# Performance work log

Hardware: AMD Instinct MI355X
Metric: run time of the kernel (lower is better)

The kernel has to match this reference:

```python
import jax, jax.numpy as jnp
import numpy as np

N_NODES = 50000


def setup_inputs() -> dict:
    key = jax.random.key(0)
    ks = jax.random.split(key, 6)
    d_in, d_out = 256, 256
    n_edges = 1_600_000
    x = jax.random.normal(ks[0], (N_NODES, d_in), dtype=jnp.float32)
    edge_index = jax.random.randint(ks[1], (2, n_edges), 0, N_NODES, dtype=jnp.int64)
    edge_attr = jax.random.normal(ks[2], (n_edges, 16), dtype=jnp.float32)  # unused by forward
    W1 = jax.random.normal(ks[3], (d_in, d_out), dtype=jnp.float32) * (1.0 / np.sqrt(d_in))
    b1 = jnp.zeros((d_out,), dtype=jnp.float32)
    W2 = jax.random.normal(ks[4], (d_out, d_out), dtype=jnp.float32) * (1.0 / np.sqrt(d_out))
    b2 = jnp.zeros((d_out,), dtype=jnp.float32)
    eps = jnp.zeros((1,), dtype=jnp.float32)  # train_eps=True, init 0
    return {"x": x, "edge_index": edge_index, "edge_attr": edge_attr,
            "W1": W1, "b1": b1, "W2": W2, "b2": b2, "eps": eps}


def reference(x, edge_index, edge_attr, W1, b1, W2, b2, eps):
    src, dst = edge_index[0], edge_index[1]
    # sum aggregation: agg[i] = sum_{(j->i) in E} x[j]
    agg = jax.ops.segment_sum(x[src], dst, num_segments=N_NODES)  # [N, d_in]
    h = (1.0 + eps[0]) * x + agg
    # MLP: Linear -> ReLU -> (dropout=0) -> Linear
    h = jax.nn.relu(h @ W1 + b1)
    out = h @ W2 + b2
    return out
```

## Files before the change

kernel.cpp:

```cpp
#include <hip/hip_runtime.h>
#include <stdint.h>

#define NODES 50000
#define D 256
#define MP 50048
#define NBUCK 196
#define CAP 10240
#define EPB 4096
#define HS_LD 264
#define CAST_BLOCKS 12500

typedef short bf16x8 __attribute__((ext_vector_type(8)));
typedef float f32x4 __attribute__((ext_vector_type(4)));

__device__ inline unsigned short f2b(float f) {
    unsigned int u = __float_as_uint(f);
    unsigned int r = (u + 0x7fffu + ((u >> 16) & 1u)) >> 16;
    return (unsigned short)r;
}

__device__ inline bool ei_is64(const int* ei) {
    return (ei[1] | ei[3] | ei[5] | ei[7]) == 0;
}
__device__ inline int ei_get(const int* __restrict__ ei, long long pos, bool is64) {
    return is64 ? ei[2 * pos] : ei[(int)pos];
}

__global__ __launch_bounds__(256) void prep_kernel(const float* __restrict__ x,
                                                   unsigned short* __restrict__ xb,
                                                   int* __restrict__ bcnt,
                                                   const float* __restrict__ W1,
                                                   const float* __restrict__ W2,
                                                   unsigned short* __restrict__ P1,
                                                   unsigned short* __restrict__ P2,
                                                   int* __restrict__ offs, int E) {
    int blk = blockIdx.x;
    if (blk < CAST_BLOCKS) {
        if (blk == 0 && threadIdx.x < NBUCK) bcnt[threadIdx.x] = 0;
        if (blk == 0 && threadIdx.x == 0) offs[NODES] = E;
        int t = blk * 256 + threadIdx.x;
        float4 v = ((const float4*)x)[t];
        unsigned int lo = (unsigned int)f2b(v.x) | ((unsigned int)f2b(v.y) << 16);
        unsigned int hi = (unsigned int)f2b(v.z) | ((unsigned int)f2b(v.w) << 16);
        ((uint2*)xb)[t] = make_uint2(lo, hi);
    } else {
        int t = (blk - CAST_BLOCKS) * 256 + threadIdx.x;
        const float* W = (t < 8192) ? W1 : W2;
        unsigned short* P = (t < 8192) ? P1 : P2;
        int u = t & 8191;
        int lane = u & 63, nt = (u >> 6) & 15, s = u >> 10;
        int q = lane >> 4, n = nt * 16 + (lane & 15);
        int kbase = s * 32 + q * 8;
#pragma unroll
        for (int j = 0; j < 8; j++) P[u * 8 + j] = f2b(W[(kbase + j) * D + n]);
    }
}

__global__ __launch_bounds__(256) void partA_kernel(const int* __restrict__ ei, int E,
                                                    int* __restrict__ bcnt,
                                                    unsigned int* __restrict__ ebufT) {
    __shared__ int cnt[256];
    __shared__ int gbase[256];
    __shared__ int lcur[256];
    bool is64 = ei_is64(ei);
    int tid = threadIdx.x;
    cnt[tid] = 0;
    lcur[tid] = 0;
    __syncthreads();
    long long pairBase = ((long long)blockIdx.x * EPB) >> 1;
    unsigned int w[16];
    int bk[16];
#pragma unroll
    for (int r = 0; r < 8; r++) {
        long long pp = pairBase + (long long)r * 256 + tid;
        long long e0 = pp * 2;
        int s0 = 0, s1 = 0, d0 = 0, d1 = 0;
        bool v1 = (e0 + 1 < E), v0 = (e0 < E);
        if (v1) {
            if (is64) {
                uint4 sv = *(const uint4*)(ei + 4 * pp);
                uint4 dv = *(const uint4*)(ei + (size_t)2 * E + 4 * pp);
                s0 = (int)sv.x; s1 = (int)sv.z; d0 = (int)dv.x; d1 = (int)dv.z;
            } else {
                uint2 sv = *(const uint2*)(ei + 2 * pp);
                uint2 dv = *(const uint2*)(ei + (size_t)E + 2 * pp);
                s0 = (int)sv.x; s1 = (int)sv.y; d0 = (int)dv.x; d1 = (int)dv.y;
            }
        } else if (v0) {
            s0 = ei_get(ei, e0, is64);
            d0 = ei_get(ei, (long long)E + e0, is64);
        }
        bk[2 * r] = v0 ? (d0 >> 8) : -1;
        bk[2 * r + 1] = v1 ? (d1 >> 8) : -1;
        w[2 * r] = ((unsigned int)(d0 & 255) << 16) | (unsigned int)s0;
        w[2 * r + 1] = ((unsigned int)(d1 & 255) << 16) | (unsigned int)s1;
        if (v0) atomicAdd(&cnt[bk[2 * r]], 1);
        if (v1) atomicAdd(&cnt[bk[2 * r + 1]], 1);
    }
    __syncthreads();
    if (tid < NBUCK && cnt[tid] > 0) gbase[tid] = atomicAdd(&bcnt[tid], cnt[tid]);
    __syncthreads();
#pragma unroll
    for (int r = 0; r < 16; r++) {
        if (bk[r] >= 0) {
            int p = atomicAdd(&lcur[bk[r]], 1);
            ebufT[(size_t)bk[r] * CAP + gbase[bk[r]] + p] = w[r];
        }
    }
}

__global__ __launch_bounds__(1024) void partB_kernel(const int* __restrict__ bcnt,
                                                     const unsigned int* __restrict__ ebufT,
                                                     int* __restrict__ offs,
                                                     int* __restrict__ ebuf) {
    __shared__ int sb[256];
    __shared__ int ncnt[2048];
    __shared__ int ncur[2048];
    __shared__ int nexcl[256];
    int b = blockIdx.x, tid = threadIdx.x;
    if (tid < 256) sb[tid] = (tid < NBUCK) ? bcnt[tid] : 0;
    for (int i = tid; i < 2048; i += 1024) ncnt[i] = 0;
    __syncthreads();
    for (int off = 1; off < 256; off <<= 1) {
        int xv = 0;
        if (tid < 256 && tid >= off) xv = sb[tid - off];
        __syncthreads();
        if (tid < 256) sb[tid] += xv;
        __syncthreads();
    }
    int n = bcnt[b];
    int base = sb[b] - n;
    const unsigned int* reg = ebufT + (size_t)b * CAP;
    for (int i = tid; i < n; i += 1024) {
        unsigned int w = reg[i];
        atomicAdd(&ncnt[((w >> 16) << 3) | ((w & 0xffffu) >> 13)], 1);
    }
    __syncthreads();
    if (tid < 256) {
        int s = 0;
#pragma unroll
        for (int c = 0; c < 8; c++) s += ncnt[tid * 8 + c];
        nexcl[tid] = s;
    }
    __syncthreads();
    for (int off = 1; off < 256; off <<= 1) {
        int xv = 0;
        if (tid < 256 && tid >= off) xv = nexcl[tid - off];
        __syncthreads();
        if (tid < 256) nexcl[tid] += xv;
        __syncthreads();
    }
    if (tid < 256) {
        int s = 0;
#pragma unroll
        for (int c = 0; c < 8; c++) s += ncnt[tid * 8 + c];
        int excl = nexcl[tid] - s;
        int node = b * 256 + tid;
        if (node < NODES) offs[node] = base + excl;
        int run = excl;
#pragma unroll
        for (int c = 0; c < 8; c++) {
            ncur[tid * 8 + c] = run;
            run += ncnt[tid * 8 + c];
        }
    }
    __syncthreads();
    for (int i = tid; i < n; i += 1024) {
        unsigned int w = reg[i];
        int p = atomicAdd(&ncur[((w >> 16) << 3) | ((w & 0xffffu) >> 13)], 1);
        ebuf[base + p] = (int)(w & 0xffffu);
    }
}

__device__ inline void upk2(uint2 w, float* a) {
    a[0] += __uint_as_float(w.x << 16);
    a[1] += __uint_as_float(w.x & 0xffff0000u);
    a[2] += __uint_as_float(w.y << 16);
    a[3] += __uint_as_float(w.y & 0xffff0000u);
}

__global__ __launch_bounds__(256) void fused_kernel(const unsigned short* __restrict__ xb,
                                                    const int* __restrict__ offs,
                                                    const int* __restrict__ ebuf,
                                                    const float* __restrict__ eps,
                                                    const unsigned short* __restrict__ P1,
                                                    const float* __restrict__ b1,
                                                    const unsigned short* __restrict__ P2,
                                                    const float* __restrict__ b2,
                                                    float* __restrict__ out, int Mvalid) {
    __shared__ unsigned short hs[64 * HS_LD];
    int wv = threadIdx.x >> 6;
    int lane = threadIdx.x & 63;
    int quad = lane >> 4, l16 = lane & 15;
    int mBase = blockIdx.x * 64;
    float scale = 1.0f + eps[0];
    const unsigned short* colBase = xb + lane * 4;

    for (int t = 0; t < 16; ++t) {
        int row = (wv << 4) + t;
        int node = mBase + row;
        float aa[4] = {0, 0, 0, 0}, bb[4] = {0, 0, 0, 0};
        if (node < NODES) {
            int beg = offs[node], end = offs[node + 1];
            int j = beg;
            for (; j + 8 <= end; j += 8) {
                int idx[8];
                uint2 g[8];
#pragma unroll
                for (int k = 0; k < 8; k++) idx[k] = ebuf[j + k];
#pragma unroll
                for (int k = 0; k < 8; k++)
                    g[k] = *(const uint2*)(colBase + (size_t)idx[k] * D);
#pragma unroll
                for (int k = 0; k < 8; k += 2) {
                    upk2(g[k], aa);
                    upk2(g[k + 1], bb);
                }
            }
            for (; j < end; ++j) {
                uint2 g = *(const uint2*)(colBase + (size_t)ebuf[j] * D);
                upk2(g, aa);
            }
            uint2 v = *(const uint2*)(colBase + (size_t)node * D);
            aa[0] += scale * __uint_as_float(v.x << 16);
            aa[1] += scale * __uint_as_float(v.x & 0xffff0000u);
            aa[2] += scale * __uint_as_float(v.y << 16);
            aa[3] += scale * __uint_as_float(v.y & 0xffff0000u);
        }
        unsigned int lo = (unsigned int)f2b(aa[0] + bb[0]) | ((unsigned int)f2b(aa[1] + bb[1]) << 16);
        unsigned int hi = (unsigned int)f2b(aa[2] + bb[2]) | ((unsigned int)f2b(aa[3] + bb[3]) << 16);
        *(uint2*)(hs + row * HS_LD + lane * 4) = make_uint2(lo, hi);
    }
    __syncthreads();

    const bf16x8* B1v = (const bf16x8*)P1;
    const bf16x8* B2v = (const bf16x8*)P2;

    {
        f32x4 acc[4][4] = {};
#pragma unroll
        for (int ks = 0; ks < 8; ks++) {
            bf16x8 af[4], bf[4];
#pragma unroll
            for (int mi = 0; mi < 4; mi++)
                af[mi] = *(const bf16x8*)(hs + (mi * 16 + l16) * HS_LD + ks * 32 + quad * 8);
#pragma unroll
            for (int ni = 0; ni < 4; ni++) bf[ni] = B1v[(ks * 16 + wv * 4 + ni) * 64 + lane];
#pragma unroll
            for (int mi = 0; mi < 4; mi++)
#pragma unroll
                for (int ni = 0; ni < 4; ni++)
                    acc[mi][ni] = __builtin_amdgcn_mfma_f32_16x16x32_bf16(af[mi], bf[ni],
                                                                          acc[mi][ni], 0, 0, 0);
        }
        __syncthreads();
#pragma unroll
        for (int mi = 0; mi < 4; mi++)
#pragma unroll
            for (int ni = 0; ni < 4; ni++) {
                int col = wv * 64 + ni * 16 + l16;
                float bs = b1[col];
#pragma unroll
                for (int r = 0; r < 4; r++) {
                    int rl = mi * 16 + quad * 4 + r;
                    hs[rl * HS_LD + col] = f2b(fmaxf(acc[mi][ni][r] + bs, 0.0f));
                }
            }
    }
    __syncthreads();

    f32x4 acc[4][4] = {};
#pragma unroll
    for (int ks = 0; ks < 8; ks++) {
        bf16x8 af[4], bf[4];
#pragma unroll
        for (int mi = 0; mi < 4; mi++)
            af[mi] = *(const bf16x8*)(hs + (mi * 16 + l16) * HS_LD + ks * 32 + quad * 8);
#pragma unroll
        for (int ni = 0; ni < 4; ni++) bf[ni] = B2v[(ks * 16 + wv * 4 + ni) * 64 + lane];
#pragma unroll
        for (int mi = 0; mi < 4; mi++)
#pragma unroll
            for (int ni = 0; ni < 4; ni++)
                acc[mi][ni] =
                    __builtin_amdgcn_mfma_f32_16x16x32_bf16(af[mi], bf[ni], acc[mi][ni], 0, 0, 0);
    }
#pragma unroll
    for (int mi = 0; mi < 4; mi++)
#pragma unroll
        for (int ni = 0; ni < 4; ni++) {
            int col = wv * 64 + ni * 16 + l16;
            float bs = b2[col];
#pragma unroll
            for (int r = 0; r < 4; r++) {
                int row = mBase + mi * 16 + quad * 4 + r;
                if (row < Mvalid) out[(size_t)row * D + col] = acc[mi][ni][r] + bs;
            }
        }
}

extern "C" void kernel_launch(void* const* d_in, const int* in_sizes, int n_in,
                              void* d_out, int out_size, void* d_ws, size_t ws_size,
                              hipStream_t stream) {
    const float* x = (const float*)d_in[0];
    const int* ei = (const int*)d_in[1];
    const float* W1 = (const float*)d_in[3];
    const float* b1 = (const float*)d_in[4];
    const float* W2 = (const float*)d_in[5];
    const float* b2 = (const float*)d_in[6];
    const float* eps = (const float*)d_in[7];
    int E = in_sizes[1] / 2;

    char* p = (char*)d_ws;
    auto alloc = [&](size_t bytes) {
        char* r = p;
        p += (bytes + 255) & ~(size_t)255;
        return r;
    };
    unsigned short* xb = (unsigned short*)alloc((size_t)MP * D * 2);
    unsigned short* P1 = (unsigned short*)alloc(8192 * 8 * 2);
    unsigned short* P2 = (unsigned short*)alloc(8192 * 8 * 2);
    int* bcnt = (int*)alloc((size_t)NBUCK * 4);
    int* offs = (int*)alloc((size_t)(NODES + 1) * 4);
    int* ebuf = (int*)alloc((size_t)E * 4);
    unsigned int* ebufT = (unsigned int*)alloc((size_t)NBUCK * CAP * 4);

    prep_kernel<<<CAST_BLOCKS + 64, 256, 0, stream>>>(x, xb, bcnt, W1, W2, P1, P2, offs, E);
    partA_kernel<<<(E + EPB - 1) / EPB, 256, 0, stream>>>(ei, E, bcnt, ebufT);
    partB_kernel<<<NBUCK, 1024, 0, stream>>>(bcnt, ebufT, offs, ebuf);
    fused_kernel<<<MP / 64, 256, 0, stream>>>(xb, offs, ebuf, eps, P1, b1, P2, b2,
                                              (float*)d_out, NODES);
}
```

Before: 434.3 us.

## Split aggregation from MLP GEMM and stage bucket scatter through shared memory

The fused gather+MLP kernel is split in two. A new aggregation kernel assigns one wave per node across many blocks and writes a bf16 intermediate h0. A GEMM-only kernel then reads its A operand directly from global memory instead of LDS. The goal is more parallelism and better latency hiding in the irregular gather, which before ran 16 nodes serially per wave over only 782 blocks. Separately, the partA bucketing kernel now sorts edges by bucket in an LDS staging buffer via a prefix scan, so global writes are contiguous per bucket. The cost is an extra global round-trip for h0 and one more kernel launch.

```diff
diff --git a/kernel.cpp b/kernel.cpp
--- a/kernel.cpp
+++ b/kernel.cpp
@@ -60,12 +60,13 @@
                                                     int* __restrict__ bcnt,
                                                     unsigned int* __restrict__ ebufT) {
     __shared__ int cnt[256];
+    __shared__ int incl[256];
+    __shared__ int lcur[256];
     __shared__ int gbase[256];
-    __shared__ int lcur[256];
+    __shared__ unsigned int stage[EPB];
     bool is64 = ei_is64(ei);
     int tid = threadIdx.x;
     cnt[tid] = 0;
-    lcur[tid] = 0;
     __syncthreads();
     long long pairBase = ((long long)blockIdx.x * EPB) >> 1;
     unsigned int w[16];
@@ -90,21 +91,40 @@
             s0 = ei_get(ei, e0, is64);
             d0 = ei_get(ei, (long long)E + e0, is64);
         }
-        bk[2 * r] = v0 ? (d0 >> 8) : -1;
-        bk[2 * r + 1] = v1 ? (d1 >> 8) : -1;
-        w[2 * r] = ((unsigned int)(d0 & 255) << 16) | (unsigned int)s0;
-        w[2 * r + 1] = ((unsigned int)(d1 & 255) << 16) | (unsigned int)s1;
-        if (v0) atomicAdd(&cnt[bk[2 * r]], 1);
-        if (v1) atomicAdd(&cnt[bk[2 * r + 1]], 1);
-    }
-    __syncthreads();
-    if (tid < NBUCK && cnt[tid] > 0) gbase[tid] = atomicAdd(&bcnt[tid], cnt[tid]);
+        bk[2 * r] = v0 ? (d0 >> 8) : 255;
+        bk[2 * r + 1] = v1 ? (d1 >> 8) : 255;
+        w[2 * r] = ((unsigned int)bk[2 * r] << 24) |
+                   ((unsigned int)(d0 & 255) << 16) | (unsigned int)s0;
+        w[2 * r + 1] = ((unsigned int)bk[2 * r + 1] << 24) |
+                       ((unsigned int)(d1 & 255) << 16) | (unsigned int)s1;
+        atomicAdd(&cnt[bk[2 * r]], 1);
+        atomicAdd(&cnt[bk[2 * r + 1]], 1);
+    }
+    __syncthreads();
+    int c = cnt[tid];
+    incl[tid] = c;
+    __syncthreads();
+    for (int off = 1; off < 256; off <<= 1) {
+        int xv = (tid >= off) ? incl[tid - off] : 0;
+        __syncthreads();
+        incl[tid] += xv;
+        __syncthreads();
+    }
+    if (tid < NBUCK && c > 0) gbase[tid] = atomicAdd(&bcnt[tid], c);
+    lcur[tid] = incl[tid] - c;
     __syncthreads();
 #pragma unroll
     for (int r = 0; r < 16; r++) {
-        if (bk[r] >= 0) {
-            int p = atomicAdd(&lcur[bk[r]], 1);
-            ebufT[(size_t)bk[r] * CAP + gbase[bk[r]] + p] = w[r];
+        int p = atomicAdd(&lcur[bk[r]], 1);
+        stage[p] = w[r];
+    }
+    __syncthreads();
+    for (int i = tid; i < EPB; i += 256) {
+        unsigned int u = stage[i];
+        int b = u >> 24;
+        if (b < NBUCK) {
+            int slot = gbase[b] + (i - (incl[b] - cnt[b]));
+            ebufT[(size_t)b * CAP + slot] = u & 0x00FFFFFFu;
         }
     }
 }
@@ -179,60 +199,71 @@
     a[3] += __uint_as_float(w.y & 0xffff0000u);
 }
 
-__global__ __launch_bounds__(256) void fused_kernel(const unsigned short* __restrict__ xb,
-                                                    const int* __restrict__ offs,
-                                                    const int* __restrict__ ebuf,
-                                                    const float* __restrict__ eps,
-                                                    const unsigned short* __restrict__ P1,
-                                                    const float* __restrict__ b1,
-                                                    const unsigned short* __restrict__ P2,
-                                                    const float* __restrict__ b2,
-                                                    float* __restrict__ out, int Mvalid) {
+__global__ __launch_bounds__(256) void agg_kernel(const unsigned short* __restrict__ xb,
+                                                  const int* __restrict__ offs,
+                                                  const int* __restrict__ ebuf,
+                                                  const float* __restrict__ eps,
+                                                  unsigned short* __restrict__ h0) {
+    int wv = (blockIdx.x * 256 + threadIdx.x) >> 6;
+    if (wv >= NODES) return;
+    int lane = threadIdx.x & 63;
+    const unsigned short* colBase = xb + lane * 4;
+    float aa[4] = {0, 0, 0, 0}, bb[4] = {0, 0, 0, 0};
+    int beg = offs[wv], end = offs[wv + 1];
+    int j = beg;
+    for (; j + 8 <= end; j += 8) {
+        int idx[8];
+        uint2 g[8];
+#pragma unroll
+        for (int k = 0; k < 8; k++) idx[k] = ebuf[j + k];
+#pragma unroll
+        for (int k = 0; k < 8; k++) g[k] = *(const uint2*)(colBase + (size_t)idx[k] * D);
+#pragma unroll
+        for (int k = 0; k < 8; k += 2) {
+            upk2(g[k], aa);
+            upk2(g[k + 1], bb);
+        }
+    }
+    if (j + 4 <= end) {
+        int idx[4];
+        uint2 g[4];
+#pragma unroll
+        for (int k = 0; k < 4; k++) idx[k] = ebuf[j + k];
+#pragma unroll
+        for (int k = 0; k < 4; k++) g[k] = *(const uint2*)(colBase + (size_t)idx[k] * D);
+#pragma unroll
+        for (int k = 0; k < 4; k += 2) {
+            upk2(g[k], aa);
+            upk2(g[k + 1], bb);
+        }
+        j += 4;
+    }
+    for (; j < end; ++j) {
+        uint2 g = *(const uint2*)(colBase + (size_t)ebuf[j] * D);
+        upk2(g, aa);
+    }
+    float scale = 1.0f + eps[0];
+    uint2 v = *(const uint2*)(colBase + (size_t)wv * D);
+    aa[0] += scale * __uint_as_float(v.x << 16);
+    aa[1] += scale * __uint_as_float(v.x & 0xffff0000u);
+    aa[2] += scale * __uint_as_float(v.y << 16);
+    aa[3] += scale * __uint_as_float(v.y & 0xffff0000u);
+    unsigned int lo = (unsigned int)f2b(aa[0] + bb[0]) | ((unsigned int)f2b(aa[1] + bb[1]) << 16);
+    unsigned int hi = (unsigned int)f2b(aa[2] + bb[2]) | ((unsigned int)f2b(aa[3] + bb[3]) << 16);
+    *(uint2*)(h0 + (size_t)wv * D + lane * 4) = make_uint2(lo, hi);
+}
+
+__global__ __launch_bounds__(256) void gemm_fused_kernel(const unsigned short* __restrict__ A,
+                                                         const unsigned short* __restrict__ P1,
+                                                         const float* __restrict__ b1,
+                                                         const unsigned short* __restrict__ P2,
+                                                         const float* __restrict__ b2,
+                                                         float* __restrict__ out, int Mvalid) {
     __shared__ unsigned short hs[64 * HS_LD];
     int wv = threadIdx.x >> 6;
     int lane = threadIdx.x & 63;
     int quad = lane >> 4, l16 = lane & 15;
     int mBase = blockIdx.x * 64;
-    float scale = 1.0f + eps[0];
-    const unsigned short* colBase = xb + lane * 4;
-
-    for (int t = 0; t < 16; ++t) {
-        int row = (wv << 4) + t;
-        int node = mBase + row;
-        float aa[4] = {0, 0, 0, 0}, bb[4] = {0, 0, 0, 0};
-        if (node < NODES) {
-            int beg = offs[node], end = offs[node + 1];
-            int j = beg;
-            for (; j + 8 <= end; j += 8) {
-                int idx[8];
-                uint2 g[8];
-#pragma unroll
-                for (int k = 0; k < 8; k++) idx[k] = ebuf[j + k];
-#pragma unroll
-                for (int k = 0; k < 8; k++)
-                    g[k] = *(const uint2*)(colBase + (size_t)idx[k] * D);
-#pragma unroll
-                for (int k = 0; k < 8; k += 2) {
-                    upk2(g[k], aa);
-                    upk2(g[k + 1], bb);
-                }
-            }
-            for (; j < end; ++j) {
-                uint2 g = *(const uint2*)(colBase + (size_t)ebuf[j] * D);
-                upk2(g, aa);
-            }
-            uint2 v = *(const uint2*)(colBase + (size_t)node * D);
-            aa[0] += scale * __uint_as_float(v.x << 16);
-            aa[1] += scale * __uint_as_float(v.x & 0xffff0000u);
-            aa[2] += scale * __uint_as_float(v.y << 16);
-            aa[3] += scale * __uint_as_float(v.y & 0xffff0000u);
-        }
-        unsigned int lo = (unsigned int)f2b(aa[0] + bb[0]) | ((unsigned int)f2b(aa[1] + bb[1]) << 16);
-        unsigned int hi = (unsigned int)f2b(aa[2] + bb[2]) | ((unsigned int)f2b(aa[3] + bb[3]) << 16);
-        *(uint2*)(hs + row * HS_LD + lane * 4) = make_uint2(lo, hi);
-    }
-    __syncthreads();
-
     const bf16x8* B1v = (const bf16x8*)P1;
     const bf16x8* B2v = (const bf16x8*)P2;
 
@@ -242,8 +273,10 @@
         for (int ks = 0; ks < 8; ks++) {
             bf16x8 af[4], bf[4];
 #pragma unroll
-            for (int mi = 0; mi < 4; mi++)
-                af[mi] = *(const bf16x8*)(hs + (mi * 16 + l16) * HS_LD + ks * 32 + quad * 8);
+            for (int mi = 0; mi < 4; mi++) {
+                int row = mBase + mi * 16 + l16;
+                af[mi] = *(const bf16x8*)(A + (size_t)row * D + ks * 32 + quad * 8);
+            }
 #pragma unroll
             for (int ni = 0; ni < 4; ni++) bf[ni] = B1v[(ks * 16 + wv * 4 + ni) * 64 + lane];
 #pragma unroll
@@ -253,7 +286,6 @@
                     acc[mi][ni] = __builtin_amdgcn_mfma_f32_16x16x32_bf16(af[mi], bf[ni],
                                                                           acc[mi][ni], 0, 0, 0);
         }
-        __syncthreads();
 #pragma unroll
         for (int mi = 0; mi < 4; mi++)
 #pragma unroll
@@ -318,6 +350,7 @@
         return r;
     };
     unsigned short* xb = (unsigned short*)alloc((size_t)MP * D * 2);
+    unsigned short* h0 = (unsigned short*)alloc((size_t)MP * D * 2);
     unsigned short* P1 = (unsigned short*)alloc(8192 * 8 * 2);
     unsigned short* P2 = (unsigned short*)alloc(8192 * 8 * 2);
     int* bcnt = (int*)alloc((size_t)NBUCK * 4);
@@ -328,6 +361,6 @@
     prep_kernel<<<CAST_BLOCKS + 64, 256, 0, stream>>>(x, xb, bcnt, W1, W2, P1, P2, offs, E);
     partA_kernel<<<(E + EPB - 1) / EPB, 256, 0, stream>>>(ei, E, bcnt, ebufT);
     partB_kernel<<<NBUCK, 1024, 0, stream>>>(bcnt, ebufT, offs, ebuf);
-    fused_kernel<<<MP / 64, 256, 0, stream>>>(xb, offs, ebuf, eps, P1, b1, P2, b2,
-                                              (float*)d_out, NODES);
-}
+    agg_kernel<<<(NODES + 3) / 4, 256, 0, stream>>>(xb, offs, ebuf, eps, h0);
+    gemm_fused_kernel<<<MP / 64, 256, 0, stream>>>(h0, P1, b1, P2, b2, (float*)d_out, NODES);
+}
```

After: 360.2 us. 1.21x faster.
